# Kernel tuning notes

Measured on AMD Instinct MI355X. Metric: run time of the kernel, lower is better.

Reference implementation:

```python
import jax, jax.numpy as jnp
import numpy as np

NEIGHBOR_NUM = 4


def reference(vertices, feature_map, sample_idx):
    # vertices: (bs, n, 3), feature_map: (bs, n, c), sample_idx: (pool_num,)
    # pairwise squared distances: ||a||^2 + ||b||^2 - 2 a.b
    inner = jnp.einsum('bnd,bmd->bnm', vertices, vertices)  # (bs, n, n)
    quad = jnp.sum(vertices * vertices, axis=2)             # (bs, n)
    distance = -2.0 * inner + quad[:, None, :] + quad[:, :, None]
    # k+1 smallest distances (self is nearest); lax.top_k finds largest, so negate
    _, neighbor_index = jax.lax.top_k(-distance, NEIGHBOR_NUM + 1)
    neighbor_index = neighbor_index[:, :, 1:]               # drop self -> (bs, n, k)
    # gather neighbor features per batch: (bs, n, k, c)
    neighbor_feature = jax.vmap(lambda f, idx: f[idx])(feature_map, neighbor_index)
    pooled_feature = jnp.max(neighbor_feature, axis=2)      # (bs, n, c)
    vertices_pool = vertices[:, sample_idx, :]              # (bs, pool_num, 3)
    feature_map_pool = pooled_feature[:, sample_idx, :]     # (bs, pool_num, c)
    return vertices_pool, feature_map_pool


def setup_inputs() -> dict:
    key = jax.random.key(0)
    k1, k2 = jax.random.split(key)
    bs, n, c = 8, 4096, 256
    pool_num = n // 4
    vertices = jax.random.normal(k1, (bs, n, 3), dtype=jnp.float32)
    feature_map = jax.random.normal(k2, (bs, n, c), dtype=jnp.float32)
    sample_idx = jnp.arange(pool_num, dtype=jnp.int32)
    return {"vertices": vertices, "feature_map": feature_map, "sample_idx": sample_idx}
```

## Files before the change

kernel.cpp:

```cpp
#include <hip/hip_runtime.h>
#include <stdint.h>

#define BATCH 8
#define NPTS  4096
#define CH    256
#define QN    1024
#define SUBS  4
#define SUBN  (NPTS / SUBS)
#define ITERS (SUBN / 64)

__device__ __forceinline__ float fmul(float a, float b) { return __fmul_rn(a, b); }
__device__ __forceinline__ float fadd(float a, float b) { return __fadd_rn(a, b); }

__device__ __forceinline__ float cdist(const float4 vq, const float4 v) {
  float dot = fadd(fadd(fmul(vq.x, v.x), fmul(vq.y, v.y)), fmul(vq.z, v.z));
  return fadd(fadd(fmul(-2.0f, dot), v.w), vq.w);
}

__device__ __forceinline__ uint64_t mkkey(float d, uint32_t c) {
  uint32_t bb = __float_as_uint(d);
  bb ^= (uint32_t)((int32_t)bb >> 31) | 0x80000000u;
  return ((uint64_t)bb << 32) | c;
}

__device__ __forceinline__ void cswap(uint64_t& lo, uint64_t& hi) {
  uint64_t mn = hi < lo ? hi : lo;
  uint64_t mx = hi < lo ? lo : hi;
  lo = mn; hi = mx;
}

__device__ __forceinline__ uint64_t wave_min(uint64_t x) {
#define DPP_MIN_STEP(CTRL)                                                     \
  {                                                                            \
    uint32_t lo = (uint32_t)x, hi = (uint32_t)(x >> 32);                       \
    uint32_t rl = (uint32_t)__builtin_amdgcn_update_dpp((int)lo, (int)lo,      \
                                                        CTRL, 0xF, 0xF, false);\
    uint32_t rh = (uint32_t)__builtin_amdgcn_update_dpp((int)hi, (int)hi,      \
                                                        CTRL, 0xF, 0xF, false);\
    uint64_t o = ((uint64_t)rh << 32) | rl;                                    \
    x = o < x ? o : x;                                                         \
  }
  DPP_MIN_STEP(0x121)
  DPP_MIN_STEP(0x122)
  DPP_MIN_STEP(0x124)
  DPP_MIN_STEP(0x128)
#undef DPP_MIN_STEP
  { uint64_t o = (uint64_t)__shfl_xor((long long)x, 16, 64); x = o < x ? o : x; }
  { uint64_t o = (uint64_t)__shfl_xor((long long)x, 32, 64); x = o < x ? o : x; }
  return x;
}

__global__ __launch_bounds__(256) void prep_kernel(
    const float* __restrict__ verts,
    float4*      __restrict__ vc)
{
  const int p = blockIdx.x * 256 + threadIdx.x;
  const float x = verts[p * 3 + 0];
  const float y = verts[p * 3 + 1];
  const float z = verts[p * 3 + 2];
  const float q = fadd(fadd(fmul(x, x), fmul(y, y)), fmul(z, z));
  vc[p] = make_float4(x, y, z, q);
}

#define SBLOCK 512

__global__ __launch_bounds__(SBLOCK) void knn_scan_kernel(
    const float4* __restrict__ vc,
    const int*    __restrict__ sidx,
    uint64_t*     __restrict__ kbuf,
    float*        __restrict__ outV)
{
  const int W    = blockIdx.x * (SBLOCK / 64) + (threadIdx.x >> 6);
  const int lane = threadIdx.x & 63;
  const int q    = W >> 2;
  const int s    = W & (SUBS - 1);
  const int batch = q >> 10;
  const int iq    = q & (QN - 1);
  const float4* vb = vc + (size_t)batch * NPTS;
  const float4 vq = vb[sidx[iq]];

  float    d0 = __builtin_inff(), d1 = __builtin_inff(), d2 = __builtin_inff();
  uint32_t i0 = 0, i1 = 0, i2 = 0;
#pragma unroll 8
  for (int t = 0; t < ITERS; ++t) {
    const uint32_t c = s * SUBN + t * 64 + lane;
    float4 v = vb[c];
    float d = cdist(vq, v);
    bool lt = d < d2;
    d2 = lt ? d : d2;
    i2 = lt ? c : i2;
    bool s1 = d2 < d1;
    { float td = d1; uint32_t ti = i1;
      d1 = s1 ? d2 : d1;  i1 = s1 ? i2 : i1;
      d2 = s1 ? td : d2;  i2 = s1 ? ti : i2; }
    bool s0 = d1 < d0;
    { float td = d0; uint32_t ti = i0;
      d0 = s0 ? d1 : d0;  i0 = s0 ? i1 : i0;
      d1 = s0 ? td : d1;  i1 = s0 ? ti : i1; }
  }

  uint64_t k0 = mkkey(d0, i0);
  uint64_t k1 = mkkey(d1, i1);
  uint64_t k2 = mkkey(d2, i2);
  uint64_t prev = 0, l0 = 0, l1 = 0, l2 = 0, l3 = 0, l4 = 0;
#pragma unroll
  for (int r = 0; r < 5; ++r) {
    uint64_t cand = k0 > prev ? k0 : (k1 > prev ? k1 : (k2 > prev ? k2 : ~0ull));
    cand = wave_min(cand);
    if (r == 0) l0 = cand;
    if (r == 1) l1 = cand;
    if (r == 2) l2 = cand;
    if (r == 3) l3 = cand;
    if (r == 4) l4 = cand;
    prev = cand;
  }
  if (__any(k2 < l4)) {
    uint64_t b0 = ~0ull, b1 = ~0ull, b2 = ~0ull, b3 = ~0ull, b4 = ~0ull;
    for (int t = 0; t < ITERS; ++t) {
      const uint32_t c = s * SUBN + t * 64 + lane;
      uint64_t key = mkkey(cdist(vq, vb[c]), c);
      b4 = key < b4 ? key : b4;
      cswap(b3, b4); cswap(b2, b3); cswap(b1, b2); cswap(b0, b1);
    }
    prev = 0;
#pragma unroll
    for (int r = 0; r < 5; ++r) {
      uint64_t cand = b0 > prev ? b0
                    : b1 > prev ? b1
                    : b2 > prev ? b2
                    : b3 > prev ? b3
                    : b4 > prev ? b4 : ~0ull;
      cand = wave_min(cand);
      if (r == 0) l0 = cand;
      if (r == 1) l1 = cand;
      if (r == 2) l2 = cand;
      if (r == 3) l3 = cand;
      if (r == 4) l4 = cand;
      prev = cand;
    }
  }

  if (lane == 0) {
    uint64_t* kq = kbuf + (size_t)q * (SUBS * 5) + s * 5;
    kq[0] = l0; kq[1] = l1; kq[2] = l2; kq[3] = l3; kq[4] = l4;
  }
  if (s == 0 && lane < 3) {
    float val = lane == 0 ? vq.x : (lane == 1 ? vq.y : vq.z);
    outV[((size_t)batch * QN + iq) * 3 + lane] = val;
  }
}

#define GBLOCK 256
#define GQPB   (GBLOCK / 64)

__global__ __launch_bounds__(GBLOCK) void knn_gather_kernel(
    const float*    __restrict__ feat,
    const uint64_t* __restrict__ kbuf,
    float*          __restrict__ outF)
{
  const int gq   = blockIdx.x * GQPB + (threadIdx.x >> 6);
  const int lane = threadIdx.x & 63;

  uint64_t key = lane < SUBS * 5 ? kbuf[(size_t)gq * (SUBS * 5) + lane] : ~0ull;
  uint64_t prev = 0, nb1 = 0, nb2 = 0, nb3 = 0, nb4 = 0;
#pragma unroll
  for (int r = 0; r < 5; ++r) {
    uint64_t cand = key > prev ? key : ~0ull;
    cand = wave_min(cand);
    if (r == 1) nb1 = cand;
    if (r == 2) nb2 = cand;
    if (r == 3) nb3 = cand;
    if (r == 4) nb4 = cand;
    prev = cand;
  }

  const int batch = gq >> 10;
  const float* fb = feat + (size_t)batch * NPTS * CH;
  const int col = lane * 4;

  float4 f1 = *(const float4*)(fb + (size_t)(uint32_t)nb1 * CH + col);
  float4 f2 = *(const float4*)(fb + (size_t)(uint32_t)nb2 * CH + col);
  float4 f3 = *(const float4*)(fb + (size_t)(uint32_t)nb3 * CH + col);
  float4 f4 = *(const float4*)(fb + (size_t)(uint32_t)nb4 * CH + col);
  float4 r;
  r.x = fmaxf(fmaxf(f1.x, f2.x), fmaxf(f3.x, f4.x));
  r.y = fmaxf(fmaxf(f1.y, f2.y), fmaxf(f3.y, f4.y));
  r.z = fmaxf(fmaxf(f1.z, f2.z), fmaxf(f3.z, f4.z));
  r.w = fmaxf(fmaxf(f1.w, f2.w), fmaxf(f3.w, f4.w));
  *(float4*)(outF + (size_t)gq * CH + col) = r;
}

extern "C" void kernel_launch(void* const* d_in, const int* in_sizes, int n_in,
                              void* d_out, int out_size, void* d_ws, size_t ws_size,
                              hipStream_t stream) {
  const float* verts = (const float*)d_in[0];
  const float* feat  = (const float*)d_in[1];
  const int*   sidx  = (const int*)d_in[2];
  float* outV = (float*)d_out;
  float* outF = (float*)d_out + (size_t)BATCH * QN * 3;

  float4*   vc   = (float4*)d_ws;
  uint64_t* kbuf = (uint64_t*)((char*)d_ws + (size_t)BATCH * NPTS * sizeof(float4));

  prep_kernel<<<dim3(BATCH * NPTS / 256), dim3(256), 0, stream>>>(verts, vc);
  knn_scan_kernel<<<dim3(BATCH * QN * SUBS * 64 / SBLOCK), dim3(SBLOCK), 0,
                    stream>>>(vc, sidx, kbuf, outV);
  knn_gather_kernel<<<dim3(BATCH * QN / GQPB), dim3(GBLOCK), 0, stream>>>(
      feat, kbuf, outF);
}
```

Baseline: 48.02 us.

## Process four queries per wave and shrink per-lane top list to two

Each wavefront in the scan kernel now handles four query points, so every candidate vertex load is reused across four distance computations. The per-lane running list drops from three to two entries, which shrinks the insertion cost. The exact fallback rescan runs more often when a lane holds more than two true neighbours. Block size changes to 256 and launch bounds request 8 blocks per CU.

```diff
diff --git a/kernel.cpp b/kernel.cpp
--- a/kernel.cpp
+++ b/kernel.cpp
@@ -8,6 +8,7 @@
 #define SUBS  4
 #define SUBN  (NPTS / SUBS)
 #define ITERS (SUBN / 64)
+#define QPW   4
 
 __device__ __forceinline__ float fmul(float a, float b) { return __fmul_rn(a, b); }
 __device__ __forceinline__ float fadd(float a, float b) { return __fadd_rn(a, b); }
@@ -62,9 +63,9 @@
   vc[p] = make_float4(x, y, z, q);
 }
 
-#define SBLOCK 512
-
-__global__ __launch_bounds__(SBLOCK) void knn_scan_kernel(
+#define SBLOCK 256
+
+__global__ __launch_bounds__(SBLOCK, 8) void knn_scan_kernel(
     const float4* __restrict__ vc,
     const int*    __restrict__ sidx,
     uint64_t*     __restrict__ kbuf,
@@ -72,64 +73,49 @@
 {
   const int W    = blockIdx.x * (SBLOCK / 64) + (threadIdx.x >> 6);
   const int lane = threadIdx.x & 63;
-  const int q    = W >> 2;
   const int s    = W & (SUBS - 1);
-  const int batch = q >> 10;
-  const int iq    = q & (QN - 1);
+  const int qg   = W >> 2;
+  const int batch  = qg >> 8;
+  const int iqbase = (qg << 2) & (QN - 1);
   const float4* vb = vc + (size_t)batch * NPTS;
-  const float4 vq = vb[sidx[iq]];
-
-  float    d0 = __builtin_inff(), d1 = __builtin_inff(), d2 = __builtin_inff();
-  uint32_t i0 = 0, i1 = 0, i2 = 0;
-#pragma unroll 8
+
+  float4 vq[QPW];
+#pragma unroll
+  for (int j = 0; j < QPW; ++j) vq[j] = vb[sidx[iqbase + j]];
+
+  float    d0[QPW], d1[QPW];
+  uint32_t i0[QPW], i1[QPW];
+#pragma unroll
+  for (int j = 0; j < QPW; ++j) {
+    d0[j] = __builtin_inff(); d1[j] = __builtin_inff();
+    i0[j] = 0; i1[j] = 0;
+  }
+
+#pragma unroll 4
   for (int t = 0; t < ITERS; ++t) {
     const uint32_t c = s * SUBN + t * 64 + lane;
     float4 v = vb[c];
-    float d = cdist(vq, v);
-    bool lt = d < d2;
-    d2 = lt ? d : d2;
-    i2 = lt ? c : i2;
-    bool s1 = d2 < d1;
-    { float td = d1; uint32_t ti = i1;
-      d1 = s1 ? d2 : d1;  i1 = s1 ? i2 : i1;
-      d2 = s1 ? td : d2;  i2 = s1 ? ti : i2; }
-    bool s0 = d1 < d0;
-    { float td = d0; uint32_t ti = i0;
-      d0 = s0 ? d1 : d0;  i0 = s0 ? i1 : i0;
-      d1 = s0 ? td : d1;  i1 = s0 ? ti : i1; }
-  }
-
-  uint64_t k0 = mkkey(d0, i0);
-  uint64_t k1 = mkkey(d1, i1);
-  uint64_t k2 = mkkey(d2, i2);
-  uint64_t prev = 0, l0 = 0, l1 = 0, l2 = 0, l3 = 0, l4 = 0;
-#pragma unroll
-  for (int r = 0; r < 5; ++r) {
-    uint64_t cand = k0 > prev ? k0 : (k1 > prev ? k1 : (k2 > prev ? k2 : ~0ull));
-    cand = wave_min(cand);
-    if (r == 0) l0 = cand;
-    if (r == 1) l1 = cand;
-    if (r == 2) l2 = cand;
-    if (r == 3) l3 = cand;
-    if (r == 4) l4 = cand;
-    prev = cand;
-  }
-  if (__any(k2 < l4)) {
-    uint64_t b0 = ~0ull, b1 = ~0ull, b2 = ~0ull, b3 = ~0ull, b4 = ~0ull;
-    for (int t = 0; t < ITERS; ++t) {
-      const uint32_t c = s * SUBN + t * 64 + lane;
-      uint64_t key = mkkey(cdist(vq, vb[c]), c);
-      b4 = key < b4 ? key : b4;
-      cswap(b3, b4); cswap(b2, b3); cswap(b1, b2); cswap(b0, b1);
-    }
-    prev = 0;
+#pragma unroll
+    for (int j = 0; j < QPW; ++j) {
+      float d = cdist(vq[j], v);
+      bool lt = d < d1[j];
+      d1[j] = lt ? d : d1[j];
+      i1[j] = lt ? c : i1[j];
+      bool sw = d1[j] < d0[j];
+      float    td = d0[j];  uint32_t ti = i0[j];
+      d0[j] = sw ? d1[j] : d0[j];  i0[j] = sw ? i1[j] : i0[j];
+      d1[j] = sw ? td    : d1[j];  i1[j] = sw ? ti    : i1[j];
+    }
+  }
+
+#pragma unroll
+  for (int j = 0; j < QPW; ++j) {
+    uint64_t k0 = mkkey(d0[j], i0[j]);
+    uint64_t k1 = mkkey(d1[j], i1[j]);
+    uint64_t prev = 0, l0 = 0, l1 = 0, l2 = 0, l3 = 0, l4 = 0;
 #pragma unroll
     for (int r = 0; r < 5; ++r) {
-      uint64_t cand = b0 > prev ? b0
-                    : b1 > prev ? b1
-                    : b2 > prev ? b2
-                    : b3 > prev ? b3
-                    : b4 > prev ? b4 : ~0ull;
+      uint64_t cand = k0 > prev ? k0 : (k1 > prev ? k1 : ~0ull);
       cand = wave_min(cand);
       if (r == 0) l0 = cand;
       if (r == 1) l1 = cand;
@@ -138,15 +124,43 @@
       if (r == 4) l4 = cand;
       prev = cand;
     }
-  }
-
-  if (lane == 0) {
-    uint64_t* kq = kbuf + (size_t)q * (SUBS * 5) + s * 5;
-    kq[0] = l0; kq[1] = l1; kq[2] = l2; kq[3] = l3; kq[4] = l4;
-  }
+    if (__any(k1 < l4)) {
+      uint64_t b0 = ~0ull, b1 = ~0ull, b2 = ~0ull, b3 = ~0ull, b4 = ~0ull;
+      for (int t = 0; t < ITERS; ++t) {
+        const uint32_t c = s * SUBN + t * 64 + lane;
+        uint64_t key = mkkey(cdist(vq[j], vb[c]), c);
+        b4 = key < b4 ? key : b4;
+        cswap(b3, b4); cswap(b2, b3); cswap(b1, b2); cswap(b0, b1);
+      }
+      prev = 0;
+#pragma unroll
+      for (int r = 0; r < 5; ++r) {
+        uint64_t cand = b0 > prev ? b0
+                      : b1 > prev ? b1
+                      : b2 > prev ? b2
+                      : b3 > prev ? b3
+                      : b4 > prev ? b4 : ~0ull;
+        cand = wave_min(cand);
+        if (r == 0) l0 = cand;
+        if (r == 1) l1 = cand;
+        if (r == 2) l2 = cand;
+        if (r == 3) l3 = cand;
+        if (r == 4) l4 = cand;
+        prev = cand;
+      }
+    }
+    if (lane == 0) {
+      uint64_t* kq = kbuf + ((size_t)(batch * QN + iqbase + j)) * (SUBS * 5) + s * 5;
+      kq[0] = l0; kq[1] = l1; kq[2] = l2; kq[3] = l3; kq[4] = l4;
+    }
+  }
+
   if (s == 0 && lane < 3) {
-    float val = lane == 0 ? vq.x : (lane == 1 ? vq.y : vq.z);
-    outV[((size_t)batch * QN + iq) * 3 + lane] = val;
+#pragma unroll
+    for (int j = 0; j < QPW; ++j) {
+      float val = lane == 0 ? vq[j].x : (lane == 1 ? vq[j].y : vq[j].z);
+      outV[((size_t)batch * QN + iqbase + j) * 3 + lane] = val;
+    }
   }
 }
 
@@ -203,8 +217,8 @@
   uint64_t* kbuf = (uint64_t*)((char*)d_ws + (size_t)BATCH * NPTS * sizeof(float4));
 
   prep_kernel<<<dim3(BATCH * NPTS / 256), dim3(256), 0, stream>>>(verts, vc);
-  knn_scan_kernel<<<dim3(BATCH * QN * SUBS * 64 / SBLOCK), dim3(SBLOCK), 0,
-                    stream>>>(vc, sidx, kbuf, outV);
+  knn_scan_kernel<<<dim3((BATCH * QN / QPW) * SUBS / (SBLOCK / 64)),
+                    dim3(SBLOCK), 0, stream>>>(vc, sidx, kbuf, outV);
   knn_gather_kernel<<<dim3(BATCH * QN / GQPB), dim3(GBLOCK), 0, stream>>>(
       feat, kbuf, outF);
 }
```

Result: slower. 57.88 us (+20.5%).
